# Optimization experiments

Hardware: AMD Instinct MI355X
Metric: run time of the kernel (lower is better)

The kernel has to match this reference:

```python
import jax, jax.numpy as jnp
import numpy as np

EXP = 2          # self.exp
NEG = -1e9       # mask fill value
B, N1, DIM, F = 4, 1024, 1024, 4
N = N1 + 1
NTOT = F * N     # 4100


def _normalize(x):
    # L2-normalize along last dim; also return the norm (keepdims)
    n = jnp.sqrt(jnp.sum(x * x, axis=-1, keepdims=True))
    return x / n, n


def setup_inputs() -> dict:
    key = jax.random.key(0)
    k1, k2 = jax.random.split(key)
    lhs = jax.random.normal(k1, (B, N1, DIM), dtype=jnp.float32)
    rhs = jax.random.normal(k2, (B, NTOT, DIM), dtype=jnp.float32)
    return {"lhs": lhs, "rhs": rhs}


def reference(lhs, rhs):
    b, n1, dim = lhs.shape
    n = n1 + 1
    ntot = rhs.shape[1]
    f = ntot // n

    lhs_n, lhs_norm = _normalize(lhs)          # (B,N1,D), (B,N1,1)
    rhs_n, _ = _normalize(rhs)                 # (B,Ntot,D)

    # cosine similarity GEMM + power epilogue
    sim = jnp.einsum('bnd,bmd->bnm', lhs_n, rhs_n) ** EXP   # (B,N1,Ntot)

    # view as (B, N1, F, N); torch masks:
    #   sim4[..., -N1:][~eye] = -1e9   (off-diagonal of last N1 cols)
    #   sim4[..., 0] = -1e9            (first col of each frame)
    # net keep condition: j == i + 1
    sim4 = sim.reshape(b, n1, f, n)
    i = jnp.arange(n1)[:, None, None]   # (N1,1,1)
    j = jnp.arange(n)[None, None, :]    # (1,1,N)
    keep = (j == i + 1)                 # (N1,1,N), broadcasts over F
    sim4 = jnp.where(keep, sim4, jnp.float32(NEG))

    return sim4.reshape(b, n1, ntot), lhs_norm
```

## Files before the change

kernel.cpp:

```cpp
#include <hip/hip_runtime.h>

#define BB   4
#define N1   1024
#define DIM  1024
#define FF   4
#define NN   1025
#define NTOT (FF * NN)
#define SIM_TOTAL ((size_t)BB * N1 * NTOT)
#define NEGV (-1e9f)

__device__ __forceinline__ float wave_reduce_sum(float v) {
#pragma unroll
    for (int off = 32; off > 0; off >>= 1)
        v += __shfl_down(v, off, 64);
    return v;
}

__global__ __launch_bounds__(256)
void lcs_kernel(const float* __restrict__ lhs,
                const float* __restrict__ rhs,
                float* __restrict__ out) {
    const int row = blockIdx.x;
    const int b   = row >> 10;
    const int i   = row & (N1 - 1);
    const int tid = threadIdx.x;

    const float4* lrow = (const float4*)(lhs + (size_t)row * DIM);
    const float4 lv = lrow[tid];
    float p_l2 = lv.x * lv.x + lv.y * lv.y + lv.z * lv.z + lv.w * lv.w;

    float p_dot[FF], p_r2[FF];
#pragma unroll
    for (int f = 0; f < FF; ++f) {
        const size_t rrow_idx = (size_t)b * NTOT + (size_t)f * NN + (i + 1);
        const float4* rrow = (const float4*)(rhs + rrow_idx * DIM);
        const float4 rv = rrow[tid];
        p_dot[f] = lv.x * rv.x + lv.y * rv.y + lv.z * rv.z + lv.w * rv.w;
        p_r2[f]  = rv.x * rv.x + rv.y * rv.y + rv.z * rv.z + rv.w * rv.w;
    }

    float4* orow4 = (float4*)(out + (size_t)row * NTOT);
    const float4 negv = make_float4(NEGV, NEGV, NEGV, NEGV);
#pragma unroll
    for (int k = tid; k < NTOT / 4; k += 256)
        orow4[k] = negv;

    float vals[9];
    vals[0] = p_l2;
#pragma unroll
    for (int f = 0; f < FF; ++f) {
        vals[1 + 2 * f] = p_dot[f];
        vals[2 + 2 * f] = p_r2[f];
    }

    __shared__ float red[4][9];
    const int wave = tid >> 6;
    const int lane = tid & 63;
#pragma unroll
    for (int q = 0; q < 9; ++q) {
        const float r = wave_reduce_sum(vals[q]);
        if (lane == 0) red[wave][q] = r;
    }
    __syncthreads();

    if (tid == 0) {
        float s[9];
#pragma unroll
        for (int q = 0; q < 9; ++q)
            s[q] = red[0][q] + red[1][q] + red[2][q] + red[3][q];

        const float l2 = s[0];
        float* orow = out + (size_t)row * NTOT;
#pragma unroll
        for (int f = 0; f < FF; ++f) {
            const float dot = s[1 + 2 * f];
            const float r2  = s[2 + 2 * f];
            orow[f * NN + i + 1] = (dot * dot) / (l2 * r2);
        }
        out[SIM_TOTAL + row] = sqrtf(l2);
    }
}

extern "C" void kernel_launch(void* const* d_in, const int* in_sizes, int n_in,
                              void* d_out, int out_size, void* d_ws, size_t ws_size,
                              hipStream_t stream) {
    const float* lhs = (const float*)d_in[0];
    const float* rhs = (const float*)d_in[1];
    float* out = (float*)d_out;

    lcs_kernel<<<BB * N1, 256, 0, stream>>>(lhs, rhs, out);
}
```

Baseline: 126.5 us.

## Map one wave per row with nontemporal loads/stores and shuffle-only reduction

Each 64-lane wave now handles a whole output row (four rows per block), so the reduction uses only xor shuffles and needs no shared memory or block barrier. Loads of lhs/rhs and the bulk -1e9 fill use nontemporal builtins to avoid polluting cache with streaming data. The fill is issued before the loads, and an explicit vmcnt(0) wait keeps the diagonal writes ordered after the fill stores to the same row. This trades per-thread register pressure (more loads in flight per lane) for fewer blocks and less synchronization.

```diff
diff --git a/kernel.cpp b/kernel.cpp
--- a/kernel.cpp
+++ b/kernel.cpp
@@ -9,75 +9,81 @@
 #define SIM_TOTAL ((size_t)BB * N1 * NTOT)
 #define NEGV (-1e9f)
 
-__device__ __forceinline__ float wave_reduce_sum(float v) {
-#pragma unroll
-    for (int off = 32; off > 0; off >>= 1)
-        v += __shfl_down(v, off, 64);
-    return v;
-}
+typedef float f4 __attribute__((ext_vector_type(4)));
+
+__device__ __forceinline__ f4 nt_load(const f4* p)  { return __builtin_nontemporal_load(p); }
+__device__ __forceinline__ void nt_store(f4* p, f4 v) { __builtin_nontemporal_store(v, p); }
 
 __global__ __launch_bounds__(256)
 void lcs_kernel(const float* __restrict__ lhs,
                 const float* __restrict__ rhs,
                 float* __restrict__ out) {
-    const int row = blockIdx.x;
-    const int b   = row >> 10;
-    const int i   = row & (N1 - 1);
-    const int tid = threadIdx.x;
+    const int lane = threadIdx.x & 63;
+    const int row  = (blockIdx.x << 2) | (threadIdx.x >> 6);
+    const int b    = row >> 10;
+    const int i    = row & (N1 - 1);
 
-    const float4* lrow = (const float4*)(lhs + (size_t)row * DIM);
-    const float4 lv = lrow[tid];
-    float p_l2 = lv.x * lv.x + lv.y * lv.y + lv.z * lv.z + lv.w * lv.w;
+    f4* orow4 = (f4*)(out + (size_t)row * NTOT);
+    const f4 negv = { NEGV, NEGV, NEGV, NEGV };
+#pragma unroll
+    for (int c = 0; c < 16; ++c)
+        nt_store(orow4 + lane + 64 * c, negv);
+    if (lane == 0)
+        nt_store(orow4 + 1024, negv);
 
-    float p_dot[FF], p_r2[FF];
+    const f4* lrow = (const f4*)(lhs + (size_t)row * DIM);
+    f4 lv[4];
+#pragma unroll
+    for (int c = 0; c < 4; ++c)
+        lv[c] = nt_load(lrow + lane + 64 * c);
+
+    float l2 = 0.f;
+#pragma unroll
+    for (int c = 0; c < 4; ++c)
+        l2 += lv[c].x * lv[c].x + lv[c].y * lv[c].y
+            + lv[c].z * lv[c].z + lv[c].w * lv[c].w;
+
+    float dot[FF], r2[FF];
 #pragma unroll
     for (int f = 0; f < FF; ++f) {
         const size_t rrow_idx = (size_t)b * NTOT + (size_t)f * NN + (i + 1);
-        const float4* rrow = (const float4*)(rhs + rrow_idx * DIM);
-        const float4 rv = rrow[tid];
-        p_dot[f] = lv.x * rv.x + lv.y * rv.y + lv.z * rv.z + lv.w * rv.w;
-        p_r2[f]  = rv.x * rv.x + rv.y * rv.y + rv.z * rv.z + rv.w * rv.w;
+        const f4* rrow = (const f4*)(rhs + rrow_idx * DIM);
+        float d = 0.f, r = 0.f;
+#pragma unroll
+        for (int c = 0; c < 4; ++c) {
+            const f4 rv = nt_load(rrow + lane + 64 * c);
+            d += lv[c].x * rv.x + lv[c].y * rv.y + lv[c].z * rv.z + lv[c].w * rv.w;
+            r += rv.x * rv.x + rv.y * rv.y + rv.z * rv.z + rv.w * rv.w;
+        }
+        dot[f] = d;
+        r2[f]  = r;
     }
 
-    float4* orow4 = (float4*)(out + (size_t)row * NTOT);
-    const float4 negv = make_float4(NEGV, NEGV, NEGV, NEGV);
-#pragma unroll
-    for (int k = tid; k < NTOT / 4; k += 256)
-        orow4[k] = negv;
-
     float vals[9];
-    vals[0] = p_l2;
+    vals[0] = l2;
 #pragma unroll
     for (int f = 0; f < FF; ++f) {
-        vals[1 + 2 * f] = p_dot[f];
-        vals[2 + 2 * f] = p_r2[f];
+        vals[1 + 2 * f] = dot[f];
+        vals[2 + 2 * f] = r2[f];
+    }
+#pragma unroll
+    for (int q = 0; q < 9; ++q) {
+#pragma unroll
+        for (int off = 32; off > 0; off >>= 1)
+            vals[q] += __shfl_xor(vals[q], off, 64);
     }
 
-    __shared__ float red[4][9];
-    const int wave = tid >> 6;
-    const int lane = tid & 63;
-#pragma unroll
-    for (int q = 0; q < 9; ++q) {
-        const float r = wave_reduce_sum(vals[q]);
-        if (lane == 0) red[wave][q] = r;
-    }
-    __syncthreads();
-
-    if (tid == 0) {
-        float s[9];
-#pragma unroll
-        for (int q = 0; q < 9; ++q)
-            s[q] = red[0][q] + red[1][q] + red[2][q] + red[3][q];
-
-        const float l2 = s[0];
+    asm volatile("s_waitcnt vmcnt(0)" ::: "memory");
+    if (lane == 0) {
+        const float l2s = vals[0];
         float* orow = out + (size_t)row * NTOT;
 #pragma unroll
         for (int f = 0; f < FF; ++f) {
-            const float dot = s[1 + 2 * f];
-            const float r2  = s[2 + 2 * f];
-            orow[f * NN + i + 1] = (dot * dot) / (l2 * r2);
+            const float d = vals[1 + 2 * f];
+            const float r = vals[2 + 2 * f];
+            orow[f * NN + i + 1] = (d * d) / (l2s * r);
         }
-        out[SIM_TOTAL + row] = sqrtf(l2);
+        out[SIM_TOTAL + row] = sqrtf(l2s);
     }
 }
 
@@ -88,5 +94,5 @@
     const float* rhs = (const float*)d_in[1];
     float* out = (float*)d_out;
 
-    lcs_kernel<<<BB * N1, 256, 0, stream>>>(lhs, rhs, out);
+    lcs_kernel<<<BB * N1 / 4, 256, 0, stream>>>(lhs, rhs, out);
 }
```

Result: slower. 129.3 us (+2.2%).
